# Optimization experiments

Hardware: AMD Instinct MI355X
Metric: run time of the kernel (lower is better)

The kernel has to match this reference:

```python
import jax, jax.numpy as jnp
import numpy as np

DILATIONS = [1, 2, 4]


def _lstm_cell(x, h, c, W_ih, W_hh, b_ih, b_hh):
    # PyTorch LSTMCell: gates in i, f, g, o order
    gates = x @ W_ih.T + b_ih + h @ W_hh.T + b_hh
    i, f, g, o = jnp.split(gates, 4, axis=-1)
    c_new = jax.nn.sigmoid(f) * c + jax.nn.sigmoid(i) * jnp.tanh(g)
    h_new = jax.nn.sigmoid(o) * jnp.tanh(c_new)
    return h_new, c_new


def _drnn_forward(x, params):
    B, T, _ = x.shape
    H = params[0][1].shape[1]
    L = len(params)
    # static per-(t, layer) update mask from dilations
    masks = jnp.asarray(
        np.array([[t % d == 0 for d in DILATIONS] for t in range(T)], dtype=bool)
    )  # [T, L]

    hs0 = tuple(jnp.zeros((B, H), x.dtype) for _ in range(L))
    cs0 = tuple(jnp.zeros((B, H), x.dtype) for _ in range(L))

    def step(carry, inp):
        hs, cs = carry
        x_t, m = inp  # x_t: [B, F], m: [L] bool
        hs = list(hs)
        cs = list(cs)
        for l, (Wi, Wh, bi, bh) in enumerate(params):
            inp_l = x_t if l == 0 else hs[l - 1]
            h_new, c_new = _lstm_cell(inp_l, hs[l], cs[l], Wi, Wh, bi, bh)
            hs[l] = jnp.where(m[l], h_new, hs[l])
            cs[l] = jnp.where(m[l], c_new, cs[l])
        return (tuple(hs), tuple(cs)), hs[-1]

    _, ys = jax.lax.scan(step, (hs0, cs0), (jnp.swapaxes(x, 0, 1), masks))
    return jnp.swapaxes(ys, 0, 1)  # [B, T, H]


def setup_inputs() -> dict:
    key = jax.random.key(0)
    ks = jax.random.split(key, 16)
    B, T, F, H = 128, 1024, 128, 256
    k = 1.0 / np.sqrt(H)  # torch LSTMCell init scale

    def u(kk, shape):
        return jax.random.uniform(kk, shape, jnp.float32, -k, k)

    inp = {"x": jax.random.normal(ks[0], (B, T, F), jnp.float32)}
    in_sizes = [F, H, H]
    ki = 1
    for l in range(3):
        inp[f"W_ih{l}"] = u(ks[ki], (4 * H, in_sizes[l])); ki += 1
        inp[f"W_hh{l}"] = u(ks[ki], (4 * H, H)); ki += 1
        inp[f"b_ih{l}"] = u(ks[ki], (4 * H,)); ki += 1
        inp[f"b_hh{l}"] = u(ks[ki], (4 * H,)); ki += 1
    return inp


def reference(x, W_ih0, W_hh0, b_ih0, b_hh0,
              W_ih1, W_hh1, b_ih1, b_hh1,
              W_ih2, W_hh2, b_ih2, b_hh2):
    params = [
        (W_ih0, W_hh0, b_ih0, b_hh0),
        (W_ih1, W_hh1, b_ih1, b_hh1),
        (W_ih2, W_hh2, b_ih2, b_hh2),
    ]
    return _drnn_forward(x, params)
```

## Files before the change

### kernel.cpp

```cpp
#include <hip/hip_runtime.h>
#include <hip/hip_fp16.h>
#include <stdint.h>
#include <stddef.h>


typedef _Float16 f16;
typedef _Float16 v2h __attribute__((ext_vector_type(2)));
typedef _Float16 v8h __attribute__((ext_vector_type(8)));
typedef __fp16 h2_raw __attribute__((ext_vector_type(2)));
typedef __fp16 h8_raw __attribute__((ext_vector_type(8)));
typedef float v4f __attribute__((ext_vector_type(4)));
typedef unsigned long long u64;

#define DEVINL static __device__ __forceinline__

DEVINL float sigm(float x) { return 1.0f / (1.0f + __expf(-x)); }
DEVINL float tanh_(float x) {
  x = fminf(fmaxf(x, -15.0f), 15.0f);
  float e = __expf(-2.0f * x);
  return (1.0f - e) / (1.0f + e);
}
DEVINL v2h pack2(float a, float b) {
  return __builtin_bit_cast(v2h, __builtin_amdgcn_cvt_pkrtz(a, b));
}
DEVINL v2h bcast_pair(v2h v, int l) {
  int i = __builtin_bit_cast(int, v);
  i = __builtin_amdgcn_readlane(i, l);
  return __builtin_bit_cast(v2h, i);
}
DEVINL float fdot2(v2h a, v2h b, float c) {
  return __builtin_amdgcn_fdot2(__builtin_bit_cast(h2_raw, a),
                                __builtin_bit_cast(h2_raw, b), c, false);
}
DEVINL v4f mfma_16x16x32(v8h a, v8h b, v4f c) {
  return __builtin_amdgcn_mfma_f32_16x16x32_f16(__builtin_bit_cast(h8_raw, a),
                                                __builtin_bit_cast(h8_raw, b), c,
                                                0, 0, 0);
}


__global__ void k_cvt_x(const float2* __restrict__ src, v2h* __restrict__ dst, int n2) {
  int i = blockIdx.x * blockDim.x + threadIdx.x;
  int st = gridDim.x * blockDim.x;
  for (; i < n2; i += st) {
    float2 v = src[i];
    dst[i] = pack2(v.x, v.y);
  }
}

__global__ void k_prep_w(const float* __restrict__ wih0, const float* __restrict__ whh0,
                         const float* __restrict__ wih1, const float* __restrict__ whh1,
                         const float* __restrict__ wih2, const float* __restrict__ whh2,
                         const float* __restrict__ bi0, const float* __restrict__ bh0,
                         const float* __restrict__ bi1, const float* __restrict__ bh1,
                         const float* __restrict__ bi2, const float* __restrict__ bh2,
                         f16* wih0f, f16* whh0f, f16* wih1f, f16* whh1f,
                         f16* wih2f, f16* whh2f,
                         float* bias0, float* bias1, float* bias2) {
  int i = blockIdx.x * blockDim.x + threadIdx.x;
  if (i < 131072) wih0f[i] = (f16)wih0[i];
  whh0f[i] = (f16)whh0[i];
  wih1f[i] = (f16)wih1[i];
  whh1f[i] = (f16)whh1[i];
  wih2f[i] = (f16)wih2[i];
  whh2f[i] = (f16)whh2[i];
  if (i < 1024) {
    bias0[i] = bi0[i] + bh0[i];
    bias1[i] = bi1[i] + bh1[i];
    bias2[i] = bi2[i] + bh2[i];
  }
}


template <int K>
__launch_bounds__(256)
__global__ void k_gemm(const f16* __restrict__ A, int Tb, int t0,
                       const f16* __restrict__ W, const float* __restrict__ bias,
                       f16* __restrict__ G) {
  constexpr int LDK = K + 8;
  __shared__ f16 As[64 * LDK];
  int b = blockIdx.x >> 2, tb = blockIdx.x & 3;
  const f16* Ablk = A + ((size_t)b * Tb + t0 + tb * 64) * K;
  int tid = threadIdx.x;

  constexpr int NV = 64 * K / 8;
  const uint4* src = (const uint4*)Ablk;
  for (int i = tid; i < NV; i += 256) {
    int e = i * 8;
    int r = e / K, c0 = e % K;
    *(uint4*)&As[r * LDK + c0] = src[i];
  }
  __syncthreads();

  int wave = tid >> 6, lane = tid & 63;
  int lm = lane & 15, lk = (lane >> 4) * 8;

  v8h af[K / 32];
#pragma unroll
  for (int kc = 0; kc < K / 32; ++kc)
    af[kc] = *(const v8h*)&As[(wave * 16 + lm) * LDK + kc * 32 + lk];

  size_t grow0 = (size_t)b * 256 + tb * 64 + wave * 16;
  for (int nt = 0; nt < 64; ++nt) {
    v4f acc = {0.0f, 0.0f, 0.0f, 0.0f};
    const f16* Wrow = W + (size_t)(nt * 16 + lm) * K + lk;
#pragma unroll
    for (int kc = 0; kc < K / 32; ++kc) {
      v8h bf = *(const v8h*)(Wrow + kc * 32);
      acc = mfma_16x16x32(af[kc], bf, acc);
    }
    float bv = bias[nt * 16 + lm];
#pragma unroll
    for (int r = 0; r < 4; ++r) {
      int m = (lane >> 4) * 4 + r;
      G[(grow0 + m) * 1024 + nt * 16 + lm] = (f16)(acc[r] + bv);
    }
  }
}


template <int LAYER>
__launch_bounds__(512, 2)
__global__ void k_rec(const f16* __restrict__ G,
                      const f16* __restrict__ Whh,
                      int t0, int steps,
                      f16* __restrict__ Hout, float* __restrict__ y,
                      float* __restrict__ hstate, float* __restrict__ cstate,
                      u64* hxw) {
  int blk = blockIdx.x;
  int b = blk >> 1, half = blk & 1;
  int tid = threadIdx.x;
  int lane = tid & 63;
  int g = tid >> 7, j = tid & 127;
  int col = g * 256 + half * 128 + j;

  __shared__ float gbuf[512];
  __shared__ uint32_t hbufw[64];

  v2h w0[64], w1[64];
  {
    const v8h* wown = (const v8h*)(Whh + (size_t)col * 256 + half * 128);
    const v8h* woth = (const v8h*)(Whh + (size_t)col * 256 + (1 - half) * 128);
#pragma unroll
    for (int i = 0; i < 16; ++i) {
      v8h qa = wown[i], qb = woth[i];
#pragma unroll
      for (int p = 0; p < 4; ++p) {
        v2h ta, tb;
        ta[0] = qa[2 * p]; ta[1] = qa[2 * p + 1];
        tb[0] = qb[2 * p]; tb[1] = qb[2 * p + 1];
        w0[i * 4 + p] = ta;
        w1[i * 4 + p] = tb;
      }
    }
  }

  u64* myw = hxw + (size_t)(b * 2 + half) * 128;
  const u64* pw = hxw + (size_t)(b * 2 + (1 - half)) * 128;

  float c_st = 0.0f, last_h = 0.0f;
  v2h hp_own = pack2(0.0f, 0.0f), hp_oth = pack2(0.0f, 0.0f);

  if (t0 > 0) {
    float2 a = *(const float2*)&hstate[b * 256 + half * 128 + 2 * lane];
    hp_own = pack2(a.x, a.y);
    if (tid < 128) {
      last_h = hstate[b * 256 + half * 128 + tid];
      c_st = cstate[b * 256 + half * 128 + tid];
    }
  }

  const f16* Gp = G + (size_t)b * 256 * 1024 + col;
  float gcur = (float)Gp[0];

  for (int s = 0; s < steps; ++s) {
    int t = t0 + s;

    const u64* pwp = pw + (((t - 1) & 1) << 6) + lane;
    u64 wp = 0;
    if (t > 0)
      wp = __hip_atomic_load(pwp, __ATOMIC_RELAXED, __HIP_MEMORY_SCOPE_AGENT);
    float gnext = (s + 1 < steps) ? (float)Gp[(size_t)(s + 1) << 10] : 0.0f;

    float acc = gcur;
#pragma unroll
    for (int kk = 0; kk < 64; ++kk)
      acc = fdot2(w0[kk], bcast_pair(hp_own, kk), acc);

    if (t > 0) {
      while ((int)(wp >> 32) < t)
        wp = __hip_atomic_load(pwp, __ATOMIC_RELAXED, __HIP_MEMORY_SCOPE_AGENT);
      hp_oth = __builtin_bit_cast(v2h, (uint32_t)wp);
    }

#pragma unroll
    for (int kk = 0; kk < 64; ++kk)
      acc = fdot2(w1[kk], bcast_pair(hp_oth, kk), acc);

    gbuf[tid] = acc;
    __syncthreads();

    if (tid < 128) {
      float iv = sigm(gbuf[tid]);
      float fv = sigm(gbuf[tid + 128]);
      float gv = tanh_(gbuf[tid + 256]);
      float ov = sigm(gbuf[tid + 384]);
      c_st = fv * c_st + iv * gv;
      float hnew = ov * tanh_(c_st);
      last_h = hnew;
      float hn1 = __shfl_down(hnew, 1, 64);
      if ((tid & 1) == 0) {
        uint32_t pk = __builtin_bit_cast(uint32_t, pack2(hnew, hn1));
        u64 wv = ((u64)(uint32_t)(t + 1) << 32) | (u64)pk;
        __hip_atomic_store(&myw[((t & 1) << 6) + (tid >> 1)], wv,
                           __ATOMIC_RELAXED, __HIP_MEMORY_SCOPE_AGENT);
        hbufw[tid >> 1] = pk;
      }
      if (LAYER == 0) {
        if ((t & 1) == 0)
          Hout[((size_t)b * 512 + (t >> 1)) * 256 + half * 128 + tid] = (f16)hnew;
      } else if (LAYER == 1) {
        if ((t & 1) == 0)
          Hout[((size_t)b * 256 + (t >> 1)) * 256 + half * 128 + tid] = (f16)hnew;
      } else {
        size_t base = ((size_t)b * 1024 + (size_t)t * 4) * 256 + half * 128 + tid;
        y[base] = hnew;
        y[base + 256] = hnew;
        y[base + 512] = hnew;
        y[base + 768] = hnew;
      }
    }
    __syncthreads();
    hp_own = __builtin_bit_cast(v2h, hbufw[lane]);
    gcur = gnext;
  }

  if (tid < 128) {
    hstate[b * 256 + half * 128 + tid] = last_h;
    cstate[b * 256 + half * 128 + tid] = c_st;
  }
}


extern "C" void kernel_launch(void* const* d_in, const int* in_sizes, int n_in,
                              void* d_out, int out_size, void* d_ws, size_t ws_size,
                              hipStream_t stream) {
  const float* x = (const float*)d_in[0];
  const float* wih[3] = {(const float*)d_in[1], (const float*)d_in[5], (const float*)d_in[9]};
  const float* whh[3] = {(const float*)d_in[2], (const float*)d_in[6], (const float*)d_in[10]};
  const float* bi[3] = {(const float*)d_in[3], (const float*)d_in[7], (const float*)d_in[11]};
  const float* bh[3] = {(const float*)d_in[4], (const float*)d_in[8], (const float*)d_in[12]};
  float* y = (float*)d_out;

  char* p = (char*)d_ws;
  f16* Xf = (f16*)p;        p += (size_t)16777216 * 2;
  f16* Wih0f = (f16*)p;     p += (size_t)131072 * 2;
  f16* Whh0f = (f16*)p;     p += (size_t)262144 * 2;
  f16* Wih1f = (f16*)p;     p += (size_t)262144 * 2;
  f16* Whh1f = (f16*)p;     p += (size_t)262144 * 2;
  f16* Wih2f = (f16*)p;     p += (size_t)262144 * 2;
  f16* Whh2f = (f16*)p;     p += (size_t)262144 * 2;
  float* bias0 = (float*)p; p += 4096;
  float* bias1 = (float*)p; p += 4096;
  float* bias2 = (float*)p; p += 4096;
  f16* Gbuf = (f16*)p;      p += (size_t)32768 * 1024 * 2;
  f16* H0e = (f16*)p;       p += (size_t)128 * 512 * 256 * 2;
  f16* H1q = (f16*)p;       p += (size_t)128 * 256 * 256 * 2;
  float* hstate = (float*)p; p += (size_t)128 * 256 * 4;
  float* cstate = (float*)p; p += (size_t)128 * 256 * 4;
  u64* hxw0 = (u64*)p;      p += (size_t)128 * 2 * 128 * 8;
  u64* hxw1 = (u64*)p;      p += (size_t)128 * 2 * 128 * 8;
  u64* hxw2 = (u64*)p;      p += (size_t)128 * 2 * 128 * 8;

  k_cvt_x<<<4096, 256, 0, stream>>>((const float2*)x, (v2h*)Xf, 8388608);
  k_prep_w<<<1024, 256, 0, stream>>>(wih[0], whh[0], wih[1], whh[1], wih[2], whh[2],
                                     bi[0], bh[0], bi[1], bh[1], bi[2], bh[2],
                                     Wih0f, Whh0f, Wih1f, Whh1f, Wih2f, Whh2f,
                                     bias0, bias1, bias2);

  for (int c = 0; c < 4; ++c) {
    k_gemm<128><<<512, 256, 0, stream>>>(Xf, 1024, c * 256, Wih0f, bias0, Gbuf);
    k_rec<0><<<256, 512, 0, stream>>>(Gbuf, Whh0f, c * 256, 256, H0e, nullptr,
                                      hstate, cstate, hxw0);
  }
  for (int c = 0; c < 2; ++c) {
    k_gemm<256><<<512, 256, 0, stream>>>(H0e, 512, c * 256, Wih1f, bias1, Gbuf);
    k_rec<1><<<256, 512, 0, stream>>>(Gbuf, Whh1f, c * 256, 256, H1q, nullptr,
                                      hstate, cstate, hxw1);
  }
  k_gemm<256><<<512, 256, 0, stream>>>(H1q, 256, 0, Wih2f, bias2, Gbuf);
  k_rec<2><<<256, 512, 0, stream>>>(Gbuf, Whh2f, 0, 256, nullptr, y,
                                    hstate, cstate, hxw2);
}
```

Before: 4.735 ms.

## Batch recurrence over 16-sequence groups with MFMA and tiled gate layout

The recurrent kernel moves from one sequence per block pair using fdot2 with readlane broadcasts to 16-sequence groups per block pair, computing h@Whh with 16x16x32 MFMA and holding Whh fragments in registers. Hidden state is kept in a swizzled LDS buffer. Halves exchange 16x64 packed words per step through tagged atomics, and the next step's gate preactivations are double-buffered in LDS. The input GEMM is rewritten to hold weight fragments in registers and write gates directly in the recurrence's MFMA fragment layout. The recurrence now launches only 16 blocks, so most CUs sit idle during the serial phase. The per-step exchange and synchronization now carry larger payloads.

```diff
diff --git a/kernel.cpp b/kernel.cpp
--- a/kernel.cpp
+++ b/kernel.cpp
@@ -7,7 +7,6 @@
 typedef _Float16 f16;
 typedef _Float16 v2h __attribute__((ext_vector_type(2)));
 typedef _Float16 v8h __attribute__((ext_vector_type(8)));
-typedef __fp16 h2_raw __attribute__((ext_vector_type(2)));
 typedef __fp16 h8_raw __attribute__((ext_vector_type(8)));
 typedef float v4f __attribute__((ext_vector_type(4)));
 typedef unsigned long long u64;
@@ -23,19 +22,16 @@
 DEVINL v2h pack2(float a, float b) {
   return __builtin_bit_cast(v2h, __builtin_amdgcn_cvt_pkrtz(a, b));
 }
-DEVINL v2h bcast_pair(v2h v, int l) {
-  int i = __builtin_bit_cast(int, v);
-  i = __builtin_amdgcn_readlane(i, l);
-  return __builtin_bit_cast(v2h, i);
-}
-DEVINL float fdot2(v2h a, v2h b, float c) {
-  return __builtin_amdgcn_fdot2(__builtin_bit_cast(h2_raw, a),
-                                __builtin_bit_cast(h2_raw, b), c, false);
-}
-DEVINL v4f mfma_16x16x32(v8h a, v8h b, v4f c) {
+DEVINL v4f mfma16(v8h a, v8h b, v4f c) {
   return __builtin_amdgcn_mfma_f32_16x16x32_f16(__builtin_bit_cast(h8_raw, a),
                                                 __builtin_bit_cast(h8_raw, b), c,
                                                 0, 0, 0);
+}
+DEVINL size_t goff(int g, int tloc, int hf) {
+  return ((size_t)((g * 256 + tloc) * 2 + hf)) << 13;
+}
+DEVINL int hdw(int m, int d2) {
+  return m * 128 + ((((d2 >> 2)) ^ (m & 7)) << 2) + (d2 & 3);
 }
 
 
@@ -72,48 +68,54 @@
 }
 
 
-template <int K>
-__launch_bounds__(256)
-__global__ void k_gemm(const f16* __restrict__ A, int Tb, int t0,
-                       const f16* __restrict__ W, const float* __restrict__ bias,
-                       f16* __restrict__ G) {
-  constexpr int LDK = K + 8;
-  __shared__ f16 As[64 * LDK];
-  int b = blockIdx.x >> 2, tb = blockIdx.x & 3;
-  const f16* Ablk = A + ((size_t)b * Tb + t0 + tb * 64) * K;
+template <int K, int BBW>
+__launch_bounds__(512, 2)
+__global__ void k_gemm_b(const f16* __restrict__ A, size_t gstr, size_t mstr,
+                         size_t tstr, int t0a,
+                         const f16* __restrict__ W, const float* __restrict__ bias,
+                         f16* __restrict__ G) {
+  constexpr int NCH = 8 / BBW;
+  int blk = blockIdx.x;
+  int g = blk / (32 * NCH);
+  int rem = blk % (32 * NCH);
+  int tt = rem / NCH;
+  int chBase = (rem % NCH) * 32;
   int tid = threadIdx.x;
-
-  constexpr int NV = 64 * K / 8;
-  const uint4* src = (const uint4*)Ablk;
-  for (int i = tid; i < NV; i += 256) {
-    int e = i * 8;
-    int r = e / K, c0 = e % K;
-    *(uint4*)&As[r * LDK + c0] = src[i];
-  }
-  __syncthreads();
-
-  int wave = tid >> 6, lane = tid & 63;
-  int lm = lane & 15, lk = (lane >> 4) * 8;
-
-  v8h af[K / 32];
-#pragma unroll
-  for (int kc = 0; kc < K / 32; ++kc)
-    af[kc] = *(const v8h*)&As[(wave * 16 + lm) * LDK + kc * 32 + lk];
-
-  size_t grow0 = (size_t)b * 256 + tb * 64 + wave * 16;
-  for (int nt = 0; nt < 64; ++nt) {
-    v4f acc = {0.0f, 0.0f, 0.0f, 0.0f};
-    const f16* Wrow = W + (size_t)(nt * 16 + lm) * K + lk;
-#pragma unroll
-    for (int kc = 0; kc < K / 32; ++kc) {
-      v8h bf = *(const v8h*)(Wrow + kc * 32);
-      acc = mfma_16x16x32(af[kc], bf, acc);
-    }
-    float bv = bias[nt * 16 + lm];
-#pragma unroll
-    for (int r = 0; r < 4; ++r) {
-      int m = (lane >> 4) * 4 + r;
-      G[(grow0 + m) * 1024 + nt * 16 + lm] = (f16)(acc[r] + bv);
+  int w = tid >> 6, lane = tid & 63;
+  int ln = lane & 15, quad = lane >> 4;
+
+  v8h bf[BBW][K / 32];
+  float bv[BBW];
+  int sbase[BBW];
+#pragma unroll
+  for (int p = 0; p < BBW; ++p) {
+    int bbg = chBase + w * BBW + p;
+    int col = bbg * 16 + ln;
+    bv[p] = bias[col];
+    const f16* wr = W + (size_t)col * K + quad * 8;
+#pragma unroll
+    for (int kc = 0; kc < K / 32; ++kc) bf[p][kc] = *(const v8h*)(wr + kc * 32);
+    int hf = (col >> 7) & 1, gt = col >> 8, wrk = (col >> 4) & 7;
+    sbase[p] = hf * 8192 + ((wrk * 4 + gt) * 64 + lane) * 4;
+  }
+
+  for (int i = 0; i < 8; ++i) {
+    int tloc = tt * 8 + i;
+    const f16* arow = A + (size_t)g * gstr + (size_t)ln * mstr +
+                      (size_t)(t0a + tloc) * tstr + quad * 8;
+    v8h af[K / 32];
+#pragma unroll
+    for (int kc = 0; kc < K / 32; ++kc) af[kc] = *(const v8h*)(arow + kc * 32);
+    size_t gbase = (size_t)(g * 256 + tloc) * 16384;
+#pragma unroll
+    for (int p = 0; p < BBW; ++p) {
+      v4f acc = {0.0f, 0.0f, 0.0f, 0.0f};
+#pragma unroll
+      for (int kc = 0; kc < K / 32; ++kc) acc = mfma16(af[kc], bf[p][kc], acc);
+      uint2 pk;
+      pk.x = __builtin_bit_cast(uint32_t, pack2(acc[0] + bv[p], acc[1] + bv[p]));
+      pk.y = __builtin_bit_cast(uint32_t, pack2(acc[2] + bv[p], acc[3] + bv[p]));
+      *(uint2*)(G + gbase + sbase[p]) = pk;
     }
   }
 }
@@ -121,124 +123,198 @@
 
 template <int LAYER>
 __launch_bounds__(512, 2)
-__global__ void k_rec(const f16* __restrict__ G,
-                      const f16* __restrict__ Whh,
-                      int t0, int steps,
-                      f16* __restrict__ Hout, float* __restrict__ y,
-                      float* __restrict__ hstate, float* __restrict__ cstate,
-                      u64* hxw) {
+__global__ void k_rec_b(const f16* __restrict__ Grec,
+                        const f16* __restrict__ Whh,
+                        int t0, int steps,
+                        f16* __restrict__ Hout, float* __restrict__ y,
+                        uint32_t* __restrict__ hstate32, float* __restrict__ cstate,
+                        u64* __restrict__ hxw) {
   int blk = blockIdx.x;
-  int b = blk >> 1, half = blk & 1;
+  int g = blk >> 1, hf = blk & 1;
   int tid = threadIdx.x;
-  int lane = tid & 63;
-  int g = tid >> 7, j = tid & 127;
-  int col = g * 256 + half * 128 + j;
-
-  __shared__ float gbuf[512];
-  __shared__ uint32_t hbufw[64];
-
-  v2h w0[64], w1[64];
+  int w = tid >> 6, lane = tid & 63;
+  int ln = lane & 15, quad = lane >> 4;
+
+  __shared__ uint32_t hbuf[16 * 128];
+  __shared__ f16 Gt2[2][8192];
+
+  v8h wf[4][8];
+#pragma unroll
+  for (int gt = 0; gt < 4; ++gt) {
+    int col = gt * 256 + hf * 128 + w * 16 + ln;
+    const f16* wr = Whh + (size_t)col * 256 + quad * 8;
+#pragma unroll
+    for (int kc = 0; kc < 8; ++kc) wf[gt][kc] = *(const v8h*)(wr + kc * 32);
+  }
+
+  float c_st[4];
   {
-    const v8h* wown = (const v8h*)(Whh + (size_t)col * 256 + half * 128);
-    const v8h* woth = (const v8h*)(Whh + (size_t)col * 256 + (1 - half) * 128);
-#pragma unroll
-    for (int i = 0; i < 16; ++i) {
-      v8h qa = wown[i], qb = woth[i];
-#pragma unroll
-      for (int p = 0; p < 4; ++p) {
-        v2h ta, tb;
-        ta[0] = qa[2 * p]; ta[1] = qa[2 * p + 1];
-        tb[0] = qb[2 * p]; tb[1] = qb[2 * p + 1];
-        w0[i * 4 + p] = ta;
-        w1[i * 4 + p] = tb;
+    int m = tid >> 5, u8 = tid & 31;
+    if (t0 == 0) {
+      uint4 z = {0u, 0u, 0u, 0u};
+      *(uint4*)&hbuf[m * 128 + ((u8 ^ (m & 7)) << 2)] = z;
+#pragma unroll
+      for (int r = 0; r < 4; ++r) c_st[r] = 0.0f;
+    } else {
+      uint4 v = *(const uint4*)&hstate32[(size_t)(g * 16 + m) * 128 + u8 * 4];
+      *(uint4*)&hbuf[m * 128 + ((u8 ^ (m & 7)) << 2)] = v;
+#pragma unroll
+      for (int r = 0; r < 4; ++r)
+        c_st[r] = cstate[(size_t)(g * 16 + quad * 4 + r) * 256 + hf * 128 + w * 16 + ln];
+    }
+  }
+  {
+    const uint4* src = (const uint4*)(Grec + goff(g, 0, hf));
+    uint4 a = src[tid * 2], b = src[tid * 2 + 1];
+    *(uint4*)&Gt2[0][tid * 16] = a;
+    *(uint4*)&Gt2[0][tid * 16 + 8] = b;
+  }
+  __syncthreads();
+
+  u64* myw = hxw + ((size_t)(g * 2 + hf)) * 2048;
+  const u64* pw = hxw + ((size_t)(g * 2 + (1 - hf))) * 2048;
+
+  const int rbase = (lane & 1) * 2;
+  const int dp_own = w * 8 + (ln >> 1);
+  const int wi0 = tid * 2, wi1 = wi0 + 1;
+  const int pm0 = wi0 >> 6, pm1 = wi1 >> 6;
+  const int gq0 = (1 - hf) * 64 + (wi0 & 63), gq1 = (1 - hf) * 64 + (wi1 & 63);
+  const int pdw0 = hdw(pm0, gq0), pdw1 = hdw(pm1, gq1);
+
+  uint32_t lastpk[2] = {0u, 0u};
+
+  for (int s = 0; s < steps; ++s) {
+    const int t = t0 + s;
+    const int p = s & 1;
+
+    uint4 ga, gb;
+    const bool havenext = (s + 1 < steps);
+    if (havenext) {
+      const uint4* src = (const uint4*)(Grec + goff(g, s + 1, hf));
+      ga = src[tid * 2];
+      gb = src[tid * 2 + 1];
+    }
+
+    v4f acc[4];
+#pragma unroll
+    for (int gt = 0; gt < 4; ++gt) {
+      uint2 gv = *(const uint2*)&Gt2[p][((w * 4 + gt) * 64 + lane) * 4];
+      v2h gl = __builtin_bit_cast(v2h, gv.x);
+      v2h gh = __builtin_bit_cast(v2h, gv.y);
+      acc[gt][0] = (float)gl[0];
+      acc[gt][1] = (float)gl[1];
+      acc[gt][2] = (float)gh[0];
+      acc[gt][3] = (float)gh[1];
+    }
+
+#pragma unroll
+    for (int kc4 = 0; kc4 < 4; ++kc4) {
+      int kc = hf * 4 + kc4;
+      v8h af = *(const v8h*)&hbuf[ln * 128 + (((kc * 4 + quad) ^ (ln & 7)) << 2)];
+#pragma unroll
+      for (int gt = 0; gt < 4; ++gt) acc[gt] = mfma16(af, wf[gt][kc], acc[gt]);
+    }
+
+    if (s > 0) {
+      const u64* p0 = pw + (((t - 1) & 1) << 10);
+      u64 v0 = __hip_atomic_load(p0 + wi0, __ATOMIC_RELAXED, __HIP_MEMORY_SCOPE_AGENT);
+      u64 v1 = __hip_atomic_load(p0 + wi1, __ATOMIC_RELAXED, __HIP_MEMORY_SCOPE_AGENT);
+      while (((int)(v0 >> 32) < t) || ((int)(v1 >> 32) < t)) {
+        v0 = __hip_atomic_load(p0 + wi0, __ATOMIC_RELAXED, __HIP_MEMORY_SCOPE_AGENT);
+        v1 = __hip_atomic_load(p0 + wi1, __ATOMIC_RELAXED, __HIP_MEMORY_SCOPE_AGENT);
       }
-    }
-  }
-
-  u64* myw = hxw + (size_t)(b * 2 + half) * 128;
-  const u64* pw = hxw + (size_t)(b * 2 + (1 - half)) * 128;
-
-  float c_st = 0.0f, last_h = 0.0f;
-  v2h hp_own = pack2(0.0f, 0.0f), hp_oth = pack2(0.0f, 0.0f);
-
-  if (t0 > 0) {
-    float2 a = *(const float2*)&hstate[b * 256 + half * 128 + 2 * lane];
-    hp_own = pack2(a.x, a.y);
-    if (tid < 128) {
-      last_h = hstate[b * 256 + half * 128 + tid];
-      c_st = cstate[b * 256 + half * 128 + tid];
-    }
-  }
-
-  const f16* Gp = G + (size_t)b * 256 * 1024 + col;
-  float gcur = (float)Gp[0];
-
-  for (int s = 0; s < steps; ++s) {
-    int t = t0 + s;
-
-    const u64* pwp = pw + (((t - 1) & 1) << 6) + lane;
-    u64 wp = 0;
-    if (t > 0)
-      wp = __hip_atomic_load(pwp, __ATOMIC_RELAXED, __HIP_MEMORY_SCOPE_AGENT);
-    float gnext = (s + 1 < steps) ? (float)Gp[(size_t)(s + 1) << 10] : 0.0f;
-
-    float acc = gcur;
-#pragma unroll
-    for (int kk = 0; kk < 64; ++kk)
-      acc = fdot2(w0[kk], bcast_pair(hp_own, kk), acc);
-
-    if (t > 0) {
-      while ((int)(wp >> 32) < t)
-        wp = __hip_atomic_load(pwp, __ATOMIC_RELAXED, __HIP_MEMORY_SCOPE_AGENT);
-      hp_oth = __builtin_bit_cast(v2h, (uint32_t)wp);
-    }
-
-#pragma unroll
-    for (int kk = 0; kk < 64; ++kk)
-      acc = fdot2(w1[kk], bcast_pair(hp_oth, kk), acc);
-
-    gbuf[tid] = acc;
+      hbuf[pdw0] = (uint32_t)v0;
+      hbuf[pdw1] = (uint32_t)v1;
+    }
     __syncthreads();
 
-    if (tid < 128) {
-      float iv = sigm(gbuf[tid]);
-      float fv = sigm(gbuf[tid + 128]);
-      float gv = tanh_(gbuf[tid + 256]);
-      float ov = sigm(gbuf[tid + 384]);
-      c_st = fv * c_st + iv * gv;
-      float hnew = ov * tanh_(c_st);
-      last_h = hnew;
-      float hn1 = __shfl_down(hnew, 1, 64);
-      if ((tid & 1) == 0) {
-        uint32_t pk = __builtin_bit_cast(uint32_t, pack2(hnew, hn1));
-        u64 wv = ((u64)(uint32_t)(t + 1) << 32) | (u64)pk;
-        __hip_atomic_store(&myw[((t & 1) << 6) + (tid >> 1)], wv,
-                           __ATOMIC_RELAXED, __HIP_MEMORY_SCOPE_AGENT);
-        hbufw[tid >> 1] = pk;
+#pragma unroll
+    for (int kc4 = 0; kc4 < 4; ++kc4) {
+      int kc = (1 - hf) * 4 + kc4;
+      v8h af = *(const v8h*)&hbuf[ln * 128 + (((kc * 4 + quad) ^ (ln & 7)) << 2)];
+#pragma unroll
+      for (int gt = 0; gt < 4; ++gt) acc[gt] = mfma16(af, wf[gt][kc], acc[gt]);
+    }
+
+    float hnew[4];
+#pragma unroll
+    for (int r = 0; r < 4; ++r) {
+      float iv = sigm(acc[0][r]);
+      float fv = sigm(acc[1][r]);
+      float gv = tanh_(acc[2][r]);
+      float ov = sigm(acc[3][r]);
+      c_st[r] = fv * c_st[r] + iv * gv;
+      hnew[r] = ov * tanh_(c_st[r]);
+    }
+
+    {
+      bool odd = (lane & 1) != 0;
+      float send0 = odd ? hnew[0] : hnew[2];
+      float send1 = odd ? hnew[1] : hnew[3];
+      float keep0 = odd ? hnew[2] : hnew[0];
+      float keep1 = odd ? hnew[3] : hnew[1];
+      float r0 = __shfl_xor(send0, 1, 64);
+      float r1 = __shfl_xor(send1, 1, 64);
+      v2h pr0 = odd ? pack2(r0, keep0) : pack2(keep0, r0);
+      v2h pr1 = odd ? pack2(r1, keep1) : pack2(keep1, r1);
+      uint32_t pk0 = __builtin_bit_cast(uint32_t, pr0);
+      uint32_t pk1 = __builtin_bit_cast(uint32_t, pr1);
+      int m0 = quad * 4 + rbase;
+      u64 tg = (u64)(uint32_t)(t + 1) << 32;
+      __hip_atomic_store(&myw[((size_t)(t & 1) << 10) + m0 * 64 + dp_own],
+                         tg | (u64)pk0, __ATOMIC_RELAXED, __HIP_MEMORY_SCOPE_AGENT);
+      __hip_atomic_store(&myw[((size_t)(t & 1) << 10) + (m0 + 1) * 64 + dp_own],
+                         tg | (u64)pk1, __ATOMIC_RELAXED, __HIP_MEMORY_SCOPE_AGENT);
+      hbuf[hdw(m0, hf * 64 + dp_own)] = pk0;
+      hbuf[hdw(m0 + 1, hf * 64 + dp_own)] = pk1;
+      lastpk[0] = pk0;
+      lastpk[1] = pk1;
+    }
+
+    if (LAYER == 0) {
+      if ((t & 1) == 0) {
+        int te = t >> 1;
+        size_t base = (size_t)(g * 512 + te) * 16 * 256 + hf * 128 + w * 16 + ln;
+#pragma unroll
+        for (int r = 0; r < 4; ++r)
+          Hout[base + (size_t)(quad * 4 + r) * 256] = (f16)hnew[r];
       }
-      if (LAYER == 0) {
-        if ((t & 1) == 0)
-          Hout[((size_t)b * 512 + (t >> 1)) * 256 + half * 128 + tid] = (f16)hnew;
-      } else if (LAYER == 1) {
-        if ((t & 1) == 0)
-          Hout[((size_t)b * 256 + (t >> 1)) * 256 + half * 128 + tid] = (f16)hnew;
-      } else {
-        size_t base = ((size_t)b * 1024 + (size_t)t * 4) * 256 + half * 128 + tid;
-        y[base] = hnew;
-        y[base + 256] = hnew;
-        y[base + 512] = hnew;
-        y[base + 768] = hnew;
+    } else if (LAYER == 1) {
+      if ((t & 1) == 0) {
+        int te = t >> 1;
+        size_t base = (size_t)(g * 256 + te) * 16 * 256 + hf * 128 + w * 16 + ln;
+#pragma unroll
+        for (int r = 0; r < 4; ++r)
+          Hout[base + (size_t)(quad * 4 + r) * 256] = (f16)hnew[r];
       }
+    } else {
+      size_t base = ((size_t)(g * 16) * 1024 + (size_t)t * 4) * 256 + hf * 128 + w * 16 + ln;
+#pragma unroll
+      for (int r = 0; r < 4; ++r) {
+        size_t b2 = base + (size_t)(quad * 4 + r) * 1024 * 256;
+        float hv = hnew[r];
+        y[b2] = hv;
+        y[b2 + 256] = hv;
+        y[b2 + 512] = hv;
+        y[b2 + 768] = hv;
+      }
+    }
+
+    if (havenext) {
+      *(uint4*)&Gt2[p ^ 1][tid * 16] = ga;
+      *(uint4*)&Gt2[p ^ 1][tid * 16 + 8] = gb;
     }
     __syncthreads();
-    hp_own = __builtin_bit_cast(v2h, hbufw[lane]);
-    gcur = gnext;
-  }
-
-  if (tid < 128) {
-    hstate[b * 256 + half * 128 + tid] = last_h;
-    cstate[b * 256 + half * 128 + tid] = c_st;
-  }
+  }
+
+#pragma unroll
+  for (int j = 0; j < 2; ++j) {
+    int m = quad * 4 + rbase + j;
+    hstate32[(size_t)(g * 16 + m) * 128 + hf * 64 + dp_own] = lastpk[j];
+  }
+#pragma unroll
+  for (int r = 0; r < 4; ++r)
+    cstate[(size_t)(g * 16 + quad * 4 + r) * 256 + hf * 128 + w * 16 + ln] = c_st[r];
 }
 
 
@@ -263,14 +339,14 @@
   float* bias0 = (float*)p; p += 4096;
   float* bias1 = (float*)p; p += 4096;
   float* bias2 = (float*)p; p += 4096;
-  f16* Gbuf = (f16*)p;      p += (size_t)32768 * 1024 * 2;
-  f16* H0e = (f16*)p;       p += (size_t)128 * 512 * 256 * 2;
-  f16* H1q = (f16*)p;       p += (size_t)128 * 256 * 256 * 2;
-  float* hstate = (float*)p; p += (size_t)128 * 256 * 4;
+  f16* Gbuf = (f16*)p;      p += (size_t)8 * 256 * 16384 * 2;
+  f16* H0e = (f16*)p;       p += (size_t)8 * 512 * 16 * 256 * 2;
+  f16* H1q = (f16*)p;       p += (size_t)8 * 256 * 16 * 256 * 2;
+  uint32_t* hstate32 = (uint32_t*)p; p += (size_t)128 * 128 * 4;
   float* cstate = (float*)p; p += (size_t)128 * 256 * 4;
-  u64* hxw0 = (u64*)p;      p += (size_t)128 * 2 * 128 * 8;
-  u64* hxw1 = (u64*)p;      p += (size_t)128 * 2 * 128 * 8;
-  u64* hxw2 = (u64*)p;      p += (size_t)128 * 2 * 128 * 8;
+  u64* hxw0 = (u64*)p;      p += (size_t)16 * 2048 * 8;
+  u64* hxw1 = (u64*)p;      p += (size_t)16 * 2048 * 8;
+  u64* hxw2 = (u64*)p;      p += (size_t)16 * 2048 * 8;
 
   k_cvt_x<<<4096, 256, 0, stream>>>((const float2*)x, (v2h*)Xf, 8388608);
   k_prep_w<<<1024, 256, 0, stream>>>(wih[0], whh[0], wih[1], whh[1], wih[2], whh[2],
@@ -279,16 +355,22 @@
                                      bias0, bias1, bias2);
 
   for (int c = 0; c < 4; ++c) {
-    k_gemm<128><<<512, 256, 0, stream>>>(Xf, 1024, c * 256, Wih0f, bias0, Gbuf);
-    k_rec<0><<<256, 512, 0, stream>>>(Gbuf, Whh0f, c * 256, 256, H0e, nullptr,
-                                      hstate, cstate, hxw0);
+    k_gemm_b<128, 8><<<256, 512, 0, stream>>>(Xf, (size_t)16 * 1024 * 128,
+                                              (size_t)1024 * 128, 128, c * 256,
+                                              Wih0f, bias0, Gbuf);
+    k_rec_b<0><<<16, 512, 0, stream>>>(Gbuf, Whh0f, c * 256, 256, H0e, nullptr,
+                                       hstate32, cstate, hxw0);
   }
   for (int c = 0; c < 2; ++c) {
-    k_gemm<256><<<512, 256, 0, stream>>>(H0e, 512, c * 256, Wih1f, bias1, Gbuf);
-    k_rec<1><<<256, 512, 0, stream>>>(Gbuf, Whh1f, c * 256, 256, H1q, nullptr,
-                                      hstate, cstate, hxw1);
-  }
-  k_gemm<256><<<512, 256, 0, stream>>>(H1q, 256, 0, Wih2f, bias2, Gbuf);
-  k_rec<2><<<256, 512, 0, stream>>>(Gbuf, Whh2f, 0, 256, nullptr, y,
-                                    hstate, cstate, hxw2);
-}
+    k_gemm_b<256, 4><<<512, 512, 0, stream>>>(H0e, (size_t)512 * 16 * 256,
+                                              256, (size_t)16 * 256, c * 256,
+                                              Wih1f, bias1, Gbuf);
+    k_rec_b<1><<<16, 512, 0, stream>>>(Gbuf, Whh1f, c * 256, 256, H1q, nullptr,
+                                       hstate32, cstate, hxw1);
+  }
+  k_gemm_b<256, 4><<<512, 512, 0, stream>>>(H1q, (size_t)256 * 16 * 256,
+                                            256, (size_t)16 * 256, 0,
+                                            Wih2f, bias2, Gbuf);
+  k_rec_b<2><<<16, 512, 0, stream>>>(Gbuf, Whh2f, 0, 256, nullptr, y,
+                                     hstate32, cstate, hxw2);
+}
```

Measured after the change: 16.82 ms. +255.2%, slower.
